# Performance work log

Measured on AMD Instinct MI355X. Metric: run time of the kernel, lower is better.

Reference implementation:

```python
import jax, jax.numpy as jnp
import numpy as np
from jax import lax

IN_CH = 192
CENTER_CH = 192
MID_CH = 192
K = 3
BS, H, W = 8, 64, 64
MASK_NUM = 16


def conv2d(x, w, b, padding=0, groups=1):
    # x: (N,C,H,W), w: (O, I/groups, kh, kw)
    out = lax.conv_general_dilated(
        x, w, window_strides=(1, 1),
        padding=[(padding, padding), (padding, padding)],
        dimension_numbers=('NCHW', 'OIHW', 'NCHW'),
        feature_group_count=groups)
    return out + b[None, :, None, None]


def lrelu(x):
    return jax.nn.leaky_relu(x, negative_slope=0.1)


def setup_inputs() -> dict:
    key = jax.random.key(0)
    ks = jax.random.split(key, 32)
    s = 0.02
    d = {
        'input': jax.random.normal(ks[0], (BS, IN_CH, H, W), jnp.float32),
        'list_center': jax.random.normal(ks[1], (BS, MASK_NUM, CENTER_CH), jnp.float32),
        'batch_mask': jax.random.randint(ks[2], (BS, H, W), 0, MASK_NUM),
        # self.conv: conv1x1(in,mid) -> lrelu -> conv1x1(mid,mid)
        'w0': jax.random.normal(ks[3], (MID_CH, IN_CH, 1, 1)) * s,
        'b0': jnp.zeros((MID_CH,)),
        'w1': jax.random.normal(ks[4], (MID_CH, MID_CH, 1, 1)) * s,
        'b1': jnp.zeros((MID_CH,)),
        # k_sp_gen: conv1x1(mid+center,mid), 3x3(mid,mid), depthwise 3x3(mid -> mid*k^2, groups=mid)
        'ws0': jax.random.normal(ks[5], (MID_CH, MID_CH + CENTER_CH, 1, 1)) * s,
        'bs0': jnp.zeros((MID_CH,)),
        'ws1': jax.random.normal(ks[6], (MID_CH, MID_CH, K, K)) * s,
        'bs1': jnp.zeros((MID_CH,)),
        'ws2': jax.random.normal(ks[7], (MID_CH * K * K, 1, K, K)) * s,
        'bs2': jnp.zeros((MID_CH * K * K,)),
        # k_ch_gen: GAP -> conv1x1 -> lrelu -> conv1x1 -> sigmoid
        'wc0': jax.random.normal(ks[8], (MID_CH, MID_CH, 1, 1)) * s,
        'bc0': jnp.zeros((MID_CH,)),
        'wc1': jax.random.normal(ks[9], (MID_CH, MID_CH, 1, 1)) * s,
        'bc1': jnp.zeros((MID_CH,)),
        # conv_out
        'wo': jax.random.normal(ks[10], (IN_CH, MID_CH, 1, 1)) * s,
        'bo': jnp.zeros((IN_CH,)),
    }
    return d


def mask_expand(list_center, batch_mask):
    # list_center: (bs, mask_num, ch); batch_mask: (bs, h, w) int
    # -> (bs, ch, h, w)
    gathered = jax.vmap(lambda c, m: c[m])(list_center, batch_mask)  # (bs,h,w,ch)
    return jnp.transpose(gathered, (0, 3, 1, 2))


def dynamic_conv(x, k_sp, k):
    # x: (bs, ch, h, w); k_sp: (bs, ch, k^2, h, w)
    bs, ch, h, w = x.shape
    p = (k - 1) // 2
    xp = jnp.pad(x, ((0, 0), (0, 0), (p, p), (p, p)))
    # torch Unfold ordering: kernel index = ki*k + kj, channel-major in view
    patches = jnp.stack([xp[:, :, i:i + h, j:j + w]
                         for i in range(k) for j in range(k)], axis=2)
    return jnp.einsum('bckhw,bckhw->bchw', patches, k_sp)


def reference(input, list_center, batch_mask, w0, b0, w1, b1, ws0, bs0,
              ws1, bs1, ws2, bs2, wc0, bc0, wc1, bc1, wo, bo):
    bs, _, h, w = input.shape
    k = K
    ch = MID_CH
    centers_exp = mask_expand(list_center, batch_mask)  # (bs, center_ch, h, w)
    shortcut = input
    x = conv2d(lrelu(conv2d(input, w0, b0)), w1, b1)  # self.conv
    y = jnp.concatenate([x, centers_exp], axis=1)
    y = lrelu(conv2d(y, ws0, bs0))
    y = lrelu(conv2d(y, ws1, bs1, padding=(k - 1) // 2))
    k_sp = conv2d(y, ws2, bs2, padding=(k - 1) // 2, groups=ch)
    k_sp = k_sp.reshape(bs, ch, k * k, h, w)
    out = dynamic_conv(x, k_sp, k)
    # squeeze-excite channel gate
    g = jnp.mean(out, axis=(2, 3), keepdims=True)
    g = jax.nn.sigmoid(conv2d(lrelu(conv2d(g, wc0, bc0)), wc1, bc1))
    out = g * out
    out = conv2d(out, wo, bo)
    return out + shortcut
```

## Files before the change

kernel.cpp:

```cpp
#include <hip/hip_runtime.h>
#include <hip/hip_bf16.h>

#define CH   192
#define PIX  4096
#define BSZ  8

using f32x4  = __attribute__((ext_vector_type(4))) float;
using short8 = __attribute__((ext_vector_type(8))) short;

__device__ __forceinline__ float bf2f(unsigned short u) {
    union { unsigned u32; float f; } x; x.u32 = ((unsigned)u) << 16; return x.f;
}
__device__ __forceinline__ unsigned short f2bf(float f) {
    union { float f; unsigned u; } x; x.f = f;
    unsigned u = x.u;
    unsigned r = (u + 0x7FFFu + ((u >> 16) & 1u)) >> 16;
    return (unsigned short)r;
}

__device__ __forceinline__ short8 ldsBs(const unsigned short* B, int ST, int k0, int px) {
    short8 f;
    #pragma unroll
    for (int e = 0; e < 8; ++e) f[e] = (short)B[(k0 + e) * ST + px];
    return f;
}

__global__ void k_prep_w(const float* __restrict__ w0, const float* __restrict__ w1,
                         const float* __restrict__ ws0, const float* __restrict__ wo,
                         const float* __restrict__ ws1, const float* __restrict__ lc,
                         unsigned short* __restrict__ w0f, unsigned short* __restrict__ w1f,
                         unsigned short* __restrict__ ws0xf, unsigned short* __restrict__ wof,
                         unsigned short* __restrict__ wc3f, float* __restrict__ tc) {
    int i = blockIdx.x * 256 + threadIdx.x;
    if (i < 4*36864) {
        int which = i / 36864, j = i % 36864;
        int kc = j / 6144, r = j % 6144, mf = r / 512, r2 = r % 512;
        int l = r2 >> 3, e = r2 & 7;
        int o = mf*16 + (l & 15), k = kc*32 + ((l >> 4) << 3) + e;
        float v;
        unsigned short* dst;
        if (which == 0)      { v = w0[o*192 + k];  dst = w0f;   }
        else if (which == 1) { v = w1[o*192 + k];  dst = w1f;   }
        else if (which == 2) { v = ws0[o*384 + k]; dst = ws0xf; }
        else                 { v = wo[o*192 + k];  dst = wof;   }
        dst[j] = f2bf(v);
        return;
    }
    i -= 4*36864;
    if (i < 331776) {
        int tk = i / 6144, tap = tk / 6, kc = tk % 6;
        int r = i % 6144, mf = r / 512, r2 = r % 512;
        int l = r2 >> 3, e = r2 & 7;
        int o = mf*16 + (l & 15), c = kc*32 + ((l >> 4) << 3) + e;
        wc3f[i] = f2bf(ws1[(o*192 + c)*9 + tap]);
        return;
    }
    i -= 331776;
    if (i < 24576) {
        int bm = i / 192, o = i % 192;
        const float* wr = ws0 + o*384 + 192;
        const float* cb = lc + bm*192;
        float a = 0.f;
        for (int c2 = 0; c2 < 192; ++c2) a += wr[c2] * cb[c2];
        tc[i] = a;
    }
}

__global__ __launch_bounds__(256) void k_fused3(
    const float* __restrict__ input,
    const unsigned short* __restrict__ w0f,
    const unsigned short* __restrict__ w1f,
    const unsigned short* __restrict__ ws0xf,
    const float* __restrict__ b0, const float* __restrict__ b1,
    const float* __restrict__ bs0,
    const float* __restrict__ tc, const int* __restrict__ mask,
    unsigned short* __restrict__ xg, unsigned short* __restrict__ y0t)
{
    const int b = blockIdx.y, n0 = blockIdx.x * 64;
    __shared__ unsigned short Bsm[192*66];
    __shared__ unsigned short Csm[192*67];
    const int tid = threadIdx.x, lane = tid & 63, wv = tid >> 6;
    const int li = lane & 15, kq = lane >> 4;

    {
        const float* src = input + (size_t)b*192*PIX + n0;
        #pragma unroll
        for (int j = 0; j < 6; ++j) {
            int q = tid + 256*j, k = q >> 3, g = (q & 7)*8;
            float4 v0 = *(const float4*)(src + (size_t)k*PIX + g);
            float4 v1 = *(const float4*)(src + (size_t)k*PIX + g + 4);
            unsigned d0 = f2bf(v0.x) | ((unsigned)f2bf(v0.y) << 16);
            unsigned d1 = f2bf(v0.z) | ((unsigned)f2bf(v0.w) << 16);
            unsigned d2 = f2bf(v1.x) | ((unsigned)f2bf(v1.y) << 16);
            unsigned d3 = f2bf(v1.z) | ((unsigned)f2bf(v1.w) << 16);
            unsigned* d = (unsigned*)(Bsm + k*66 + g);
            d[0]=d0; d[1]=d1; d[2]=d2; d[3]=d3;
        }
    }
    __syncthreads();

    f32x4 acc[3][4];

    #pragma unroll
    for (int m = 0; m < 3; ++m)
        #pragma unroll
        for (int n = 0; n < 4; ++n) acc[m][n] = {0.f,0.f,0.f,0.f};
    for (int kc = 0; kc < 6; ++kc) {
        short8 a[3];
        #pragma unroll
        for (int m = 0; m < 3; ++m)
            a[m] = *(const short8*)(w0f + ((kc*12 + wv*3 + m)*64 + lane)*8);
        #pragma unroll
        for (int n = 0; n < 4; ++n) {
            short8 fb = ldsBs(Bsm, 66, kc*32 + kq*8, n*16 + li);
            #pragma unroll
            for (int m = 0; m < 3; ++m)
                acc[m][n] = __builtin_amdgcn_mfma_f32_16x16x32_bf16(a[m], fb, acc[m][n], 0,0,0);
        }
    }
    #pragma unroll
    for (int m = 0; m < 3; ++m) {
        int o0 = (wv*3 + m)*16 + kq*4;
        #pragma unroll
        for (int n = 0; n < 4; ++n) {
            int px = n*16 + li;
            #pragma unroll
            for (int r = 0; r < 4; ++r) {
                float v = acc[m][n][r] + b0[o0 + r];
                v = v > 0.f ? v : 0.1f*v;
                Csm[(o0 + r)*67 + px] = f2bf(v);
            }
        }
    }
    __syncthreads();

    #pragma unroll
    for (int m = 0; m < 3; ++m)
        #pragma unroll
        for (int n = 0; n < 4; ++n) acc[m][n] = {0.f,0.f,0.f,0.f};
    for (int kc = 0; kc < 6; ++kc) {
        short8 a[3];
        #pragma unroll
        for (int m = 0; m < 3; ++m)
            a[m] = *(const short8*)(w1f + ((kc*12 + wv*3 + m)*64 + lane)*8);
        #pragma unroll
        for (int n = 0; n < 4; ++n) {
            short8 fb = ldsBs(Csm, 67, kc*32 + kq*8, n*16 + li);
            #pragma unroll
            for (int m = 0; m < 3; ++m)
                acc[m][n] = __builtin_amdgcn_mfma_f32_16x16x32_bf16(a[m], fb, acc[m][n], 0,0,0);
        }
    }
    __syncthreads();
    #pragma unroll
    for (int m = 0; m < 3; ++m) {
        int o0 = (wv*3 + m)*16 + kq*4;
        #pragma unroll
        for (int n = 0; n < 4; ++n) {
            int px = n*16 + li;
            #pragma unroll
            for (int r = 0; r < 4; ++r) {
                float v = acc[m][n][r] + b1[o0 + r];
                unsigned short h = f2bf(v);
                Bsm[(o0 + r)*66 + px] = h;
                xg[((size_t)b*192 + o0 + r)*PIX + n0 + px] = h;
            }
        }
    }
    __syncthreads();

    #pragma unroll
    for (int m = 0; m < 3; ++m)
        #pragma unroll
        for (int n = 0; n < 4; ++n) acc[m][n] = {0.f,0.f,0.f,0.f};
    for (int kc = 0; kc < 6; ++kc) {
        short8 a[3];
        #pragma unroll
        for (int m = 0; m < 3; ++m)
            a[m] = *(const short8*)(ws0xf + ((kc*12 + wv*3 + m)*64 + lane)*8);
        #pragma unroll
        for (int n = 0; n < 4; ++n) {
            short8 fb = ldsBs(Bsm, 66, kc*32 + kq*8, n*16 + li);
            #pragma unroll
            for (int m = 0; m < 3; ++m)
                acc[m][n] = __builtin_amdgcn_mfma_f32_16x16x32_bf16(a[m], fb, acc[m][n], 0,0,0);
        }
    }
    int mi_[4];
    #pragma unroll
    for (int n = 0; n < 4; ++n) mi_[n] = mask[b*PIX + n0 + n*16 + li];
    #pragma unroll
    for (int m = 0; m < 3; ++m) {
        int o0 = (wv*3 + m)*16 + kq*4;
        #pragma unroll
        for (int n = 0; n < 4; ++n) {
            int px = n*16 + li;
            const float* tcb = tc + (b*16 + mi_[n])*192;
            ushort4 w;
            unsigned short* wp = (unsigned short*)&w;
            #pragma unroll
            for (int r = 0; r < 4; ++r) {
                float v = acc[m][n][r] + bs0[o0 + r] + tcb[o0 + r];
                v = v > 0.f ? v : 0.1f*v;
                wp[r] = f2bf(v);
            }
            *(ushort4*)(Csm + px*200 + o0) = w;
        }
    }
    __syncthreads();
    #pragma unroll
    for (int j = 0; j < 6; ++j) {
        int u = tid + 256*j;
        int px = u / 24, chunk = u % 24;
        uint4 v = *(const uint4*)(Csm + px*200 + chunk*8);
        *(uint4*)(y0t + ((size_t)(b*4096 + n0 + px))*192 + chunk*8) = v;
    }
}

__global__ __launch_bounds__(512) void k_conv3t(
    const unsigned short* __restrict__ wc3f,
    const unsigned short* __restrict__ y0t,
    const float* __restrict__ bias,
    unsigned short* __restrict__ y1)
{
    const int b = blockIdx.y, h = blockIdx.x;
    __shared__ unsigned short Bs[2][3*66*40];
    const int tid = threadIdx.x, lane = tid & 63, wv = tid >> 6;
    const int li = lane & 15, kq = lane >> 4;
    const int mw = wv >> 1, nh = wv & 1;

    const int u1 = tid + 512;
    const int r0 = tid >> 2,  c0 = tid & 3;
    const int dr0 = r0/66, px0g = r0%66 - 1, hh0 = h + dr0 - 1;
    const bool ok0 = ((unsigned)hh0 < 64u) & ((unsigned)px0g < 64u);
    const size_t s0 = ok0 ? ((size_t)(b*4096 + hh0*64 + px0g))*192 + c0*8 : 0;
    const int o0f = r0*80 + c0*16;
    const int r1 = u1 >> 2,  c1 = u1 & 3;
    const int dr1 = r1/66, px1g = r1%66 - 1, hh1 = h + dr1 - 1;
    const bool act1 = (u1 < 792);
    const bool ok1 = act1 & ((unsigned)hh1 < 64u) & ((unsigned)px1g < 64u);
    const size_t s1 = ok1 ? ((size_t)(b*4096 + hh1*64 + px1g))*192 + c1*8 : 0;
    const int o1f = r1*80 + c1*16;
    const uint4 zz = {0u,0u,0u,0u};

    uint4 v0, v1;
    v0 = ok0 ? *(const uint4*)(y0t + s0) : zz;
    v1 = ok1 ? *(const uint4*)(y0t + s1) : zz;
    *(uint4*)((char*)Bs[0] + o0f) = v0;
    if (act1) *(uint4*)((char*)Bs[0] + o1f) = v1;
    __syncthreads();

    f32x4 acc[3][2];
    #pragma unroll
    for (int m = 0; m < 3; ++m)
        #pragma unroll
        for (int nn = 0; nn < 2; ++nn) acc[m][nn] = {0.f,0.f,0.f,0.f};

    for (int kc = 0; kc < 6; ++kc) {
        const int cur = kc & 1;
        if (kc < 5) {
            v0 = ok0 ? *(const uint4*)(y0t + s0 + (kc+1)*32) : zz;
            v1 = ok1 ? *(const uint4*)(y0t + s1 + (kc+1)*32) : zz;
        }
        const unsigned short* Bc = Bs[cur];
        #pragma unroll
        for (int tap = 0; tap < 9; ++tap) {
            const int dr = tap / 3, dc1 = tap % 3;
            short8 a[3];
            #pragma unroll
            for (int m = 0; m < 3; ++m)
                a[m] = *(const short8*)(wc3f + (((tap*6 + kc)*12 + mw*3 + m)*64 + lane)*8);
            #pragma unroll
            for (int nn = 0; nn < 2; ++nn) {
                int pxi = nh*32 + nn*16 + li + dc1;
                short8 fb = *(const short8*)((const char*)Bc + (dr*66 + pxi)*80 + kq*16);
                #pragma unroll
                for (int m = 0; m < 3; ++m)
                    acc[m][nn] = __builtin_amdgcn_mfma_f32_16x16x32_bf16(a[m], fb, acc[m][nn], 0,0,0);
            }
        }
        if (kc < 5) {
            *(uint4*)((char*)Bs[cur^1] + o0f) = v0;
            if (act1) *(uint4*)((char*)Bs[cur^1] + o1f) = v1;
            __syncthreads();
        }
    }

    #pragma unroll
    for (int m = 0; m < 3; ++m) {
        int oo = (mw*3 + m)*16 + kq*4;
        #pragma unroll
        for (int nn = 0; nn < 2; ++nn) {
            int px = h*64 + nh*32 + nn*16 + li;
            #pragma unroll
            for (int r = 0; r < 4; ++r) {
                float v = acc[m][nn][r] + bias[oo + r];
                v = v > 0.f ? v : 0.1f*v;
                y1[((size_t)b*192 + oo + r)*PIX + px] = f2bf(v);
            }
        }
    }
}

__global__ __launch_bounds__(256) void k_dwdyn3(
    const unsigned short* __restrict__ Y1,
    const unsigned short* __restrict__ X,
    const float* __restrict__ ws2,
    const float* __restrict__ bs2,
    unsigned short* __restrict__ OP,
    float* __restrict__ gsum)
{
    const int c = blockIdx.x, b = blockIdx.y;
    __shared__ unsigned short ysm[4096];
    __shared__ unsigned short xsm[4096];
    __shared__ float red[4];
    const int tid = threadIdx.x;
    const size_t cb = ((size_t)b*192 + c) * PIX;
    #pragma unroll
    for (int j = 0; j < 2; ++j) {
        int i = tid + 256*j;
        *(uint4*)(ysm + i*8) = *(const uint4*)(Y1 + cb + i*8);
        *(uint4*)(xsm + i*8) = *(const uint4*)(X  + cb + i*8);
    }
    float wreg[81], breg[9];
    #pragma unroll
    for (int t = 0; t < 81; ++t) wreg[t] = ws2[c*81 + t];
    #pragma unroll
    for (int t = 0; t < 9; ++t) breg[t] = bs2[c*9 + t];
    __syncthreads();

    const int w = tid & 63, rg = tid >> 6, h0 = rg * 16;
    const bool wl = (w > 0), wr = (w < 63);

    float ya[3], yb[3], yc[3], xa[3], xb[3], xc[3];
    {
        int h = h0 - 1;
        if (h >= 0) {
            int base = h*64 + w;
            ya[0] = wl ? bf2f(ysm[base-1]) : 0.f;  ya[1] = bf2f(ysm[base]);
            ya[2] = wr ? bf2f(ysm[base+1]) : 0.f;
            xa[0] = wl ? bf2f(xsm[base-1]) : 0.f;  xa[1] = bf2f(xsm[base]);
            xa[2] = wr ? bf2f(xsm[base+1]) : 0.f;
        } else { ya[0]=ya[1]=ya[2]=0.f; xa[0]=xa[1]=xa[2]=0.f; }
        int base = h0*64 + w;
        yb[0] = wl ? bf2f(ysm[base-1]) : 0.f;  yb[1] = bf2f(ysm[base]);
        yb[2] = wr ? bf2f(ysm[base+1]) : 0.f;
        xb[0] = wl ? bf2f(xsm[base-1]) : 0.f;  xb[1] = bf2f(xsm[base]);
        xb[2] = wr ? bf2f(xsm[base+1]) : 0.f;
    }

    float gacc = 0.f;
    #pragma unroll 4
    for (int j = 0; j < 16; ++j) {
        int h = h0 + j;
        if (h + 1 < 64) {
            int base = (h+1)*64 + w;
            yc[0] = wl ? bf2f(ysm[base-1]) : 0.f;  yc[1] = bf2f(ysm[base]);
            yc[2] = wr ? bf2f(ysm[base+1]) : 0.f;
            xc[0] = wl ? bf2f(xsm[base-1]) : 0.f;  xc[1] = bf2f(xsm[base]);
            xc[2] = wr ? bf2f(xsm[base+1]) : 0.f;
        } else { yc[0]=yc[1]=yc[2]=0.f; xc[0]=xc[1]=xc[2]=0.f; }

        float ksp[9];
        #pragma unroll
        for (int t = 0; t < 9; ++t) ksp[t] = breg[t];
        #pragma unroll
        for (int tj = 0; tj < 3; ++tj) {
            #pragma unroll
            for (int t = 0; t < 9; ++t) ksp[t] += ya[tj] * wreg[t*9 + tj];
            #pragma unroll
            for (int t = 0; t < 9; ++t) ksp[t] += yb[tj] * wreg[t*9 + 3 + tj];
            #pragma unroll
            for (int t = 0; t < 9; ++t) ksp[t] += yc[tj] * wreg[t*9 + 6 + tj];
        }
        float out = xa[0]*ksp[0] + xa[1]*ksp[1] + xa[2]*ksp[2]
                  + xb[0]*ksp[3] + xb[1]*ksp[4] + xb[2]*ksp[5]
                  + xc[0]*ksp[6] + xc[1]*ksp[7] + xc[2]*ksp[8];
        OP[cb + h*64 + w] = f2bf(out);
        gacc += out;
        #pragma unroll
        for (int t = 0; t < 3; ++t) {
            ya[t] = yb[t]; yb[t] = yc[t];
            xa[t] = xb[t]; xb[t] = xc[t];
        }
    }
    #pragma unroll
    for (int off = 32; off > 0; off >>= 1) gacc += __shfl_down(gacc, off);
    if ((tid & 63) == 0) red[tid >> 6] = gacc;
    __syncthreads();
    if (tid == 0) gsum[b*192 + c] = red[0] + red[1] + red[2] + red[3];
}

__global__ void k_gate(const float* __restrict__ gsum,
                       const float* __restrict__ wc0, const float* __restrict__ bc0,
                       const float* __restrict__ wc1, const float* __restrict__ bc1,
                       float* __restrict__ gvec)
{
    const int b = blockIdx.x, t = threadIdx.x;
    __shared__ float mean[192], s1[192];
    mean[t] = gsum[b*192 + t] * (1.f/4096.f);
    __syncthreads();
    float a = bc0[t];
    const float* w = wc0 + t*192;
    for (int i = 0; i < 192; ++i) a += w[i] * mean[i];
    s1[t] = a > 0.f ? a : 0.1f * a;
    __syncthreads();
    float a2 = bc1[t];
    const float* w2 = wc1 + t*192;
    for (int i = 0; i < 192; ++i) a2 += w2[i] * s1[i];
    gvec[b*192 + t] = 1.f / (1.f + __expf(-a2));
}

__global__ __launch_bounds__(256) void k_gemmo(
    const unsigned short* __restrict__ wof,
    const unsigned short* __restrict__ op,
    const float* __restrict__ bo,
    const float* __restrict__ gvec,
    const float* __restrict__ resid,
    float* __restrict__ out)
{
    const int b = blockIdx.y, n0 = blockIdx.x * 64;
    __shared__ unsigned short Bsm[192*66];
    const int tid = threadIdx.x, lane = tid & 63, wv = tid >> 6;
    const int li = lane & 15, kq = lane >> 4;

    {
        const unsigned short* src = op + (size_t)b*192*PIX + n0;
        #pragma unroll
        for (int j = 0; j < 6; ++j) {
            int q = tid + 256*j, k = q >> 3, g = (q & 7) * 8;
            uint4 v = *(const uint4*)(src + (size_t)k*PIX + g);
            float gs = gvec[b*192 + k];
            unsigned short* pv = (unsigned short*)&v;
            #pragma unroll
            for (int e = 0; e < 8; ++e) pv[e] = f2bf(bf2f(pv[e]) * gs);
            unsigned* d = (unsigned*)(Bsm + k*66 + g);
            const unsigned* s = (const unsigned*)&v;
            d[0]=s[0]; d[1]=s[1]; d[2]=s[2]; d[3]=s[3];
        }
    }
    __syncthreads();

    f32x4 acc[3][4];
    #pragma unroll
    for (int m = 0; m < 3; ++m)
        #pragma unroll
        for (int n = 0; n < 4; ++n) acc[m][n] = {0.f,0.f,0.f,0.f};
    for (int kc = 0; kc < 6; ++kc) {
        short8 a[3];
        #pragma unroll
        for (int m = 0; m < 3; ++m)
            a[m] = *(const short8*)(wof + ((kc*12 + wv*3 + m)*64 + lane)*8);
        #pragma unroll
        for (int n = 0; n < 4; ++n) {
            short8 fb = ldsBs(Bsm, 66, kc*32 + kq*8, n*16 + li);
            #pragma unroll
            for (int m = 0; m < 3; ++m)
                acc[m][n] = __builtin_amdgcn_mfma_f32_16x16x32_bf16(a[m], fb, acc[m][n], 0,0,0);
        }
    }
    #pragma unroll
    for (int m = 0; m < 3; ++m) {
        int o0 = (wv*3 + m)*16 + kq*4;
        #pragma unroll
        for (int n = 0; n < 4; ++n) {
            int px = n*16 + li;
            #pragma unroll
            for (int r = 0; r < 4; ++r) {
                size_t idx = ((size_t)b*192 + o0 + r)*PIX + n0 + px;
                out[idx] = acc[m][n][r] + bo[o0 + r] + resid[idx];
            }
        }
    }
}

extern "C" void kernel_launch(void* const* d_in, const int* in_sizes, int n_in,
                              void* d_out, int out_size, void* d_ws, size_t ws_size,
                              hipStream_t stream)
{
    const float* input = (const float*)d_in[0];
    const float* lc    = (const float*)d_in[1];
    const int*   mask  = (const int*)d_in[2];
    const float* w0  = (const float*)d_in[3];
    const float* b0  = (const float*)d_in[4];
    const float* w1  = (const float*)d_in[5];
    const float* b1  = (const float*)d_in[6];
    const float* ws0 = (const float*)d_in[7];
    const float* bs0 = (const float*)d_in[8];
    const float* ws1 = (const float*)d_in[9];
    const float* bs1 = (const float*)d_in[10];
    const float* ws2 = (const float*)d_in[11];
    const float* bs2 = (const float*)d_in[12];
    const float* wc0 = (const float*)d_in[13];
    const float* bc0 = (const float*)d_in[14];
    const float* wc1 = (const float*)d_in[15];
    const float* bc1 = (const float*)d_in[16];
    const float* wo  = (const float*)d_in[17];
    const float* bo  = (const float*)d_in[18];

    char* ws = (char*)d_ws;
    size_t off = 0;
    auto alloc = [&](size_t bytes) {
        void* p = ws + off; off = (off + bytes + 255) & ~(size_t)255; return p;
    };
    const size_t act_b = (size_t)BSZ * CH * PIX * 2;
    unsigned short* x_bf  = (unsigned short*)alloc(act_b);
    unsigned short* y0t   = (unsigned short*)alloc(act_b);
    unsigned short* y1_bf = (unsigned short*)alloc(act_b);
    unsigned short* op_bf = (unsigned short*)alloc(act_b);
    unsigned short* w0f   = (unsigned short*)alloc(36864*2);
    unsigned short* w1f   = (unsigned short*)alloc(36864*2);
    unsigned short* ws0xf = (unsigned short*)alloc(36864*2);
    unsigned short* wof   = (unsigned short*)alloc(36864*2);
    unsigned short* wc3f  = (unsigned short*)alloc(331776*2);
    float* tc   = (float*)alloc(8*16*192*4);
    float* gsum = (float*)alloc(1536*4);
    float* gvec = (float*)alloc(1536*4);

    k_prep_w<<<1968, 256, 0, stream>>>(w0, w1, ws0, wo, ws1, lc,
                                       w0f, w1f, ws0xf, wof, wc3f, tc);

    dim3 gg(64, 8);
    k_fused3<<<gg, 256, 0, stream>>>(input, w0f, w1f, ws0xf, b0, b1, bs0, tc, mask, x_bf, y0t);
    k_conv3t<<<gg, 512, 0, stream>>>(wc3f, y0t, bs1, y1_bf);
    k_dwdyn3<<<dim3(192, 8), 256, 0, stream>>>(y1_bf, x_bf, ws2, bs2, op_bf, gsum);
    k_gate<<<8, 192, 0, stream>>>(gsum, wc0, bc0, wc1, bc1, gvec);
    k_gemmo<<<gg, 256, 0, stream>>>(wof, op_bf, bo, gvec, input, (float*)d_out);
}
```

Measured before the change: 229.2 us.

## Transpose LDS activation tiles to pixel-major and fuse gate into output GEMM

Stores activation tiles in shared memory as pixel-major with a 200-element padded stride. MFMA B fragments can then be read as one 16-byte vector load instead of eight strided scalar LDS reads. The separate gate kernel is removed and its two small matvecs are recomputed redundantly in every output GEMM block, using transposed gate weights prepared once for coalesced reads. Staging stores become scattered 2-byte LDS writes, and each k_gemmo block now pays about 74K extra FMAs before its GEMM.

```diff
diff --git a/kernel.cpp b/kernel.cpp
--- a/kernel.cpp
+++ b/kernel.cpp
@@ -18,19 +18,14 @@
     return (unsigned short)r;
 }
 
-__device__ __forceinline__ short8 ldsBs(const unsigned short* B, int ST, int k0, int px) {
-    short8 f;
-    #pragma unroll
-    for (int e = 0; e < 8; ++e) f[e] = (short)B[(k0 + e) * ST + px];
-    return f;
-}
-
 __global__ void k_prep_w(const float* __restrict__ w0, const float* __restrict__ w1,
                          const float* __restrict__ ws0, const float* __restrict__ wo,
                          const float* __restrict__ ws1, const float* __restrict__ lc,
+                         const float* __restrict__ wc0, const float* __restrict__ wc1,
                          unsigned short* __restrict__ w0f, unsigned short* __restrict__ w1f,
                          unsigned short* __restrict__ ws0xf, unsigned short* __restrict__ wof,
-                         unsigned short* __restrict__ wc3f, float* __restrict__ tc) {
+                         unsigned short* __restrict__ wc3f, float* __restrict__ tc,
+                         float* __restrict__ wc0t, float* __restrict__ wc1t) {
     int i = blockIdx.x * 256 + threadIdx.x;
     if (i < 4*36864) {
         int which = i / 36864, j = i % 36864;
@@ -63,7 +58,12 @@
         float a = 0.f;
         for (int c2 = 0; c2 < 192; ++c2) a += wr[c2] * cb[c2];
         tc[i] = a;
-    }
+        return;
+    }
+    i -= 24576;
+    if (i < 36864) { int o = i / 192, c = i % 192; wc0t[c*192 + o] = wc0[o*192 + c]; return; }
+    i -= 36864;
+    if (i < 36864) { int o = i / 192, c = i % 192; wc1t[c*192 + o] = wc1[o*192 + c]; }
 }
 
 __global__ __launch_bounds__(256) void k_fused3(
@@ -77,8 +77,8 @@
     unsigned short* __restrict__ xg, unsigned short* __restrict__ y0t)
 {
     const int b = blockIdx.y, n0 = blockIdx.x * 64;
-    __shared__ unsigned short Bsm[192*66];
-    __shared__ unsigned short Csm[192*67];
+    __shared__ unsigned short Bsm[64*200];
+    __shared__ unsigned short Csm[64*200];
     const int tid = threadIdx.x, lane = tid & 63, wv = tid >> 6;
     const int li = lane & 15, kq = lane >> 4;
 
@@ -89,12 +89,14 @@
             int q = tid + 256*j, k = q >> 3, g = (q & 7)*8;
             float4 v0 = *(const float4*)(src + (size_t)k*PIX + g);
             float4 v1 = *(const float4*)(src + (size_t)k*PIX + g + 4);
-            unsigned d0 = f2bf(v0.x) | ((unsigned)f2bf(v0.y) << 16);
-            unsigned d1 = f2bf(v0.z) | ((unsigned)f2bf(v0.w) << 16);
-            unsigned d2 = f2bf(v1.x) | ((unsigned)f2bf(v1.y) << 16);
-            unsigned d3 = f2bf(v1.z) | ((unsigned)f2bf(v1.w) << 16);
-            unsigned* d = (unsigned*)(Bsm + k*66 + g);
-            d[0]=d0; d[1]=d1; d[2]=d2; d[3]=d3;
+            Bsm[(g+0)*200 + k] = f2bf(v0.x);
+            Bsm[(g+1)*200 + k] = f2bf(v0.y);
+            Bsm[(g+2)*200 + k] = f2bf(v0.z);
+            Bsm[(g+3)*200 + k] = f2bf(v0.w);
+            Bsm[(g+4)*200 + k] = f2bf(v1.x);
+            Bsm[(g+5)*200 + k] = f2bf(v1.y);
+            Bsm[(g+6)*200 + k] = f2bf(v1.z);
+            Bsm[(g+7)*200 + k] = f2bf(v1.w);
         }
     }
     __syncthreads();
@@ -112,7 +114,7 @@
             a[m] = *(const short8*)(w0f + ((kc*12 + wv*3 + m)*64 + lane)*8);
         #pragma unroll
         for (int n = 0; n < 4; ++n) {
-            short8 fb = ldsBs(Bsm, 66, kc*32 + kq*8, n*16 + li);
+            short8 fb = *(const short8*)(Bsm + (n*16 + li)*200 + kc*32 + kq*8);
             #pragma unroll
             for (int m = 0; m < 3; ++m)
                 acc[m][n] = __builtin_amdgcn_mfma_f32_16x16x32_bf16(a[m], fb, acc[m][n], 0,0,0);
@@ -124,12 +126,15 @@
         #pragma unroll
         for (int n = 0; n < 4; ++n) {
             int px = n*16 + li;
+            ushort4 w;
+            unsigned short* wp = (unsigned short*)&w;
             #pragma unroll
             for (int r = 0; r < 4; ++r) {
                 float v = acc[m][n][r] + b0[o0 + r];
                 v = v > 0.f ? v : 0.1f*v;
-                Csm[(o0 + r)*67 + px] = f2bf(v);
+                wp[r] = f2bf(v);
             }
+            *(ushort4*)(Csm + px*200 + o0) = w;
         }
     }
     __syncthreads();
@@ -145,26 +150,28 @@
             a[m] = *(const short8*)(w1f + ((kc*12 + wv*3 + m)*64 + lane)*8);
         #pragma unroll
         for (int n = 0; n < 4; ++n) {
-            short8 fb = ldsBs(Csm, 67, kc*32 + kq*8, n*16 + li);
+            short8 fb = *(const short8*)(Csm + (n*16 + li)*200 + kc*32 + kq*8);
             #pragma unroll
             for (int m = 0; m < 3; ++m)
                 acc[m][n] = __builtin_amdgcn_mfma_f32_16x16x32_bf16(a[m], fb, acc[m][n], 0,0,0);
         }
     }
-    __syncthreads();
     #pragma unroll
     for (int m = 0; m < 3; ++m) {
         int o0 = (wv*3 + m)*16 + kq*4;
         #pragma unroll
         for (int n = 0; n < 4; ++n) {
             int px = n*16 + li;
+            ushort4 w;
+            unsigned short* wp = (unsigned short*)&w;
             #pragma unroll
             for (int r = 0; r < 4; ++r) {
                 float v = acc[m][n][r] + b1[o0 + r];
                 unsigned short h = f2bf(v);
-                Bsm[(o0 + r)*66 + px] = h;
+                wp[r] = h;
                 xg[((size_t)b*192 + o0 + r)*PIX + n0 + px] = h;
             }
+            *(ushort4*)(Bsm + px*200 + o0) = w;
         }
     }
     __syncthreads();
@@ -180,7 +187,7 @@
             a[m] = *(const short8*)(ws0xf + ((kc*12 + wv*3 + m)*64 + lane)*8);
         #pragma unroll
         for (int n = 0; n < 4; ++n) {
-            short8 fb = ldsBs(Bsm, 66, kc*32 + kq*8, n*16 + li);
+            short8 fb = *(const short8*)(Bsm + (n*16 + li)*200 + kc*32 + kq*8);
             #pragma unroll
             for (int m = 0; m < 3; ++m)
                 acc[m][n] = __builtin_amdgcn_mfma_f32_16x16x32_bf16(a[m], fb, acc[m][n], 0,0,0);
@@ -391,52 +398,48 @@
     if (tid == 0) gsum[b*192 + c] = red[0] + red[1] + red[2] + red[3];
 }
 
-__global__ void k_gate(const float* __restrict__ gsum,
-                       const float* __restrict__ wc0, const float* __restrict__ bc0,
-                       const float* __restrict__ wc1, const float* __restrict__ bc1,
-                       float* __restrict__ gvec)
-{
-    const int b = blockIdx.x, t = threadIdx.x;
-    __shared__ float mean[192], s1[192];
-    mean[t] = gsum[b*192 + t] * (1.f/4096.f);
-    __syncthreads();
-    float a = bc0[t];
-    const float* w = wc0 + t*192;
-    for (int i = 0; i < 192; ++i) a += w[i] * mean[i];
-    s1[t] = a > 0.f ? a : 0.1f * a;
-    __syncthreads();
-    float a2 = bc1[t];
-    const float* w2 = wc1 + t*192;
-    for (int i = 0; i < 192; ++i) a2 += w2[i] * s1[i];
-    gvec[b*192 + t] = 1.f / (1.f + __expf(-a2));
-}
-
 __global__ __launch_bounds__(256) void k_gemmo(
     const unsigned short* __restrict__ wof,
     const unsigned short* __restrict__ op,
     const float* __restrict__ bo,
-    const float* __restrict__ gvec,
+    const float* __restrict__ gsum,
+    const float* __restrict__ wc0t, const float* __restrict__ bc0,
+    const float* __restrict__ wc1t, const float* __restrict__ bc1,
     const float* __restrict__ resid,
     float* __restrict__ out)
 {
     const int b = blockIdx.y, n0 = blockIdx.x * 64;
-    __shared__ unsigned short Bsm[192*66];
+    __shared__ unsigned short Bsm[64*200];
+    __shared__ float mean[192], s1[192], gv[192];
     const int tid = threadIdx.x, lane = tid & 63, wv = tid >> 6;
     const int li = lane & 15, kq = lane >> 4;
 
+    if (tid < 192) mean[tid] = gsum[b*192 + tid] * (1.f/4096.f);
+    __syncthreads();
+    if (tid < 192) {
+        float a = bc0[tid];
+        for (int i = 0; i < 192; ++i) a += wc0t[i*192 + tid] * mean[i];
+        s1[tid] = a > 0.f ? a : 0.1f * a;
+    }
+    __syncthreads();
+    if (tid < 192) {
+        float a2 = bc1[tid];
+        for (int i = 0; i < 192; ++i) a2 += wc1t[i*192 + tid] * s1[i];
+        gv[tid] = 1.f / (1.f + __expf(-a2));
+    }
+    __syncthreads();
+
     {
         const unsigned short* src = op + (size_t)b*192*PIX + n0;
         #pragma unroll
         for (int j = 0; j < 6; ++j) {
-            int q = tid + 256*j, k = q >> 3, g = (q & 7) * 8;
-            uint4 v = *(const uint4*)(src + (size_t)k*PIX + g);
-            float gs = gvec[b*192 + k];
-            unsigned short* pv = (unsigned short*)&v;
-            #pragma unroll
-            for (int e = 0; e < 8; ++e) pv[e] = f2bf(bf2f(pv[e]) * gs);
-            unsigned* d = (unsigned*)(Bsm + k*66 + g);
-            const unsigned* s = (const unsigned*)&v;
-            d[0]=s[0]; d[1]=s[1]; d[2]=s[2]; d[3]=s[3];
+            int q = tid + 256*j, c = q >> 3, g = (q & 7) * 8;
+            uint4 v = *(const uint4*)(src + (size_t)c*PIX + g);
+            float gs = gv[c];
+            const unsigned short* pv = (const unsigned short*)&v;
+            #pragma unroll
+            for (int e = 0; e < 8; ++e)
+                Bsm[(g+e)*200 + c] = f2bf(bf2f(pv[e]) * gs);
         }
     }
     __syncthreads();
@@ -453,7 +456,7 @@
             a[m] = *(const short8*)(wof + ((kc*12 + wv*3 + m)*64 + lane)*8);
         #pragma unroll
         for (int n = 0; n < 4; ++n) {
-            short8 fb = ldsBs(Bsm, 66, kc*32 + kq*8, n*16 + li);
+            short8 fb = *(const short8*)(Bsm + (n*16 + li)*200 + kc*32 + kq*8);
             #pragma unroll
             for (int m = 0; m < 3; ++m)
                 acc[m][n] = __builtin_amdgcn_mfma_f32_16x16x32_bf16(a[m], fb, acc[m][n], 0,0,0);
@@ -513,17 +516,18 @@
     unsigned short* ws0xf = (unsigned short*)alloc(36864*2);
     unsigned short* wof   = (unsigned short*)alloc(36864*2);
     unsigned short* wc3f  = (unsigned short*)alloc(331776*2);
-    float* tc   = (float*)alloc(8*16*192*4);
-    float* gsum = (float*)alloc(1536*4);
-    float* gvec = (float*)alloc(1536*4);
-
-    k_prep_w<<<1968, 256, 0, stream>>>(w0, w1, ws0, wo, ws1, lc,
-                                       w0f, w1f, ws0xf, wof, wc3f, tc);
+    float* tc    = (float*)alloc(8*16*192*4);
+    float* gsum  = (float*)alloc(1536*4);
+    float* wc0t  = (float*)alloc(36864*4);
+    float* wc1t  = (float*)alloc(36864*4);
+
+    k_prep_w<<<2256, 256, 0, stream>>>(w0, w1, ws0, wo, ws1, lc, wc0, wc1,
+                                       w0f, w1f, ws0xf, wof, wc3f, tc, wc0t, wc1t);
 
     dim3 gg(64, 8);
     k_fused3<<<gg, 256, 0, stream>>>(input, w0f, w1f, ws0xf, b0, b1, bs0, tc, mask, x_bf, y0t);
     k_conv3t<<<gg, 512, 0, stream>>>(wc3f, y0t, bs1, y1_bf);
     k_dwdyn3<<<dim3(192, 8), 256, 0, stream>>>(y1_bf, x_bf, ws2, bs2, op_bf, gsum);
-    k_gate<<<8, 192, 0, stream>>>(gsum, wc0, bc0, wc1, bc1, gvec);
-    k_gemmo<<<gg, 256, 0, stream>>>(wof, op_bf, bo, gvec, input, (float*)d_out);
-}
+    k_gemmo<<<gg, 256, 0, stream>>>(wof, op_bf, bo, gsum, wc0t, bc0, wc1t, bc1,
+                                    input, (float*)d_out);
+}
```

Result: faster. 218.8 us (-4.5%).
